# Kernel optimization log

Hardware: AMD Instinct MI355X
Metric: run time of the kernel (lower is better)

Reference implementation:

```python
import jax, jax.numpy as jnp
import numpy as np

B, C, P, GH, GW = 32, 3, 32, 8, 16
DIM, DEPTH, HEADS, DHEAD = 1024, 12, 16, 64
N = GH * GW              # 128 tokens
PATCH_DIM = C * P * P    # 3072
INNER = HEADS * DHEAD    # 1024
EPS = 1e-5


def layer_norm(x, g, b):
    mu = jnp.mean(x, axis=-1, keepdims=True)
    var = jnp.var(x, axis=-1, keepdims=True)
    return (x - mu) * jax.lax.rsqrt(var + EPS) * g + b


def setup_inputs() -> dict:
    key = jax.random.key(0)
    ks = iter(jax.random.split(key, 32))
    s = 0.02
    inp = {
        "img": jax.random.normal(next(ks), (B, C, GH * P, GW * P), jnp.float32),
        "sph_pos": jax.random.uniform(next(ks), (GH, GW, 2), jnp.float32),
        "sph_dist": jax.random.uniform(next(ks), (N, N), jnp.float32),
        # patch embedding conv (kernel == stride == patch)
        "conv_w": jax.random.normal(next(ks), (DIM, C, P, P), jnp.float32) * s,
        "conv_b": jnp.zeros((DIM,), jnp.float32),
        # norm_linear: LN -> Linear(dim,dim) -> LN
        "nl_ln1_g": jnp.ones((DIM,), jnp.float32),
        "nl_ln1_b": jnp.zeros((DIM,), jnp.float32),
        "nl_w": jax.random.normal(next(ks), (DIM, DIM), jnp.float32) * s,
        "nl_b": jnp.zeros((DIM,), jnp.float32),
        "nl_ln2_g": jnp.ones((DIM,), jnp.float32),
        "nl_ln2_b": jnp.zeros((DIM,), jnp.float32),
        # pos embedding Linear(2, dim)
        "pos_w": jax.random.normal(next(ks), (2, DIM), jnp.float32) * s,
        "pos_b": jnp.zeros((DIM,), jnp.float32),
        # per-layer attention params, stacked over depth
        "ln_g": jnp.ones((DEPTH, DIM), jnp.float32),
        "ln_b": jnp.zeros((DEPTH, DIM), jnp.float32),
        "wqkv": jax.random.normal(next(ks), (DEPTH, DIM, 3 * INNER), jnp.float32) * s,
        "wo": jax.random.normal(next(ks), (DEPTH, INNER, DIM), jnp.float32) * s,
        "wo_b": jnp.zeros((DEPTH, DIM), jnp.float32),
        # final transformer LN
        "tr_ln_g": jnp.ones((DIM,), jnp.float32),
        "tr_ln_b": jnp.zeros((DIM,), jnp.float32),
        # expand head: Linear(dim, patch_dim) + LN(patch_dim)
        "exp_w": jax.random.normal(next(ks), (DIM, PATCH_DIM), jnp.float32) * s,
        "exp_b": jnp.zeros((PATCH_DIM,), jnp.float32),
        "out_ln_g": jnp.ones((PATCH_DIM,), jnp.float32),
        "out_ln_b": jnp.zeros((PATCH_DIM,), jnp.float32),
    }
    return inp


def _forward(img, sph_pos, sph_dist, conv_w, conv_b, nl_ln1_g, nl_ln1_b, nl_w,
             nl_b, nl_ln2_g, nl_ln2_b, pos_w, pos_b, ln_g, ln_b, wqkv, wo,
             wo_b, tr_ln_g, tr_ln_b, exp_w, exp_b, out_ln_g, out_ln_b):
    b = img.shape[0]
    scale = DHEAD ** -0.5
    # patch embedding: Conv2d(kernel=stride=P) == per-patch linear
    patches = img.reshape(b, C, GH, P, GW, P)  # b c h p w q
    x = jnp.einsum('bchpwq,dcpq->bhwd', patches, conv_w) + conv_b  # [b,GH,GW,dim]
    x = x.reshape(b, N, DIM)
    # norm_linear
    x = layer_norm(x, nl_ln1_g, nl_ln1_b)
    x = x @ nl_w + nl_b
    x = layer_norm(x, nl_ln2_g, nl_ln2_b)
    # spherical positional embedding
    pos = (sph_pos @ pos_w + pos_b).reshape(N, DIM)
    x = x + pos[None]
    # transformer: GlobalSphereAttention blocks with residuals
    bias = 1.0 + sph_dist  # [N,N]
    for l in range(DEPTH):
        h = layer_norm(x, ln_g[l], ln_b[l])
        qkv = h @ wqkv[l]  # [b,n,3*inner]
        q, k, v = jnp.split(qkv, 3, axis=-1)
        q = q.reshape(b, N, HEADS, DHEAD).transpose(0, 2, 1, 3)
        k = k.reshape(b, N, HEADS, DHEAD).transpose(0, 2, 1, 3)
        v = v.reshape(b, N, HEADS, DHEAD).transpose(0, 2, 1, 3)
        dots = jnp.einsum('bhid,bhjd->bhij', q, k) * scale
        w = dots * bias  # broadcast over b,h
        # cross-head standardization (torch.std -> ddof=1)
        mu = jnp.mean(w, axis=1, keepdims=True)
        sd = jnp.std(w, axis=1, keepdims=True, ddof=1)
        attn = jax.nn.softmax((w - mu) / sd, axis=-1)
        o = jnp.einsum('bhij,bhjd->bhid', attn, v)
        o = o.transpose(0, 2, 1, 3).reshape(b, N, INNER)
        x = o @ wo[l] + wo_b[l] + x
    x = layer_norm(x, tr_ln_g, tr_ln_b)
    # expand and reassemble image: 'b (h w) (p1 p2 c) -> b c (h p1) (w p2)'
    x = layer_norm(x @ exp_w + exp_b, out_ln_g, out_ln_b)  # [b,N,patch_dim]
    x = x.reshape(b, GH, GW, P, P, C)
    x = x.transpose(0, 5, 1, 3, 2, 4).reshape(b, C, GH * P, GW * P)
    return x


def reference(img, sph_pos, sph_dist, conv_w, conv_b, nl_ln1_g, nl_ln1_b, nl_w,
              nl_b, nl_ln2_g, nl_ln2_b, pos_w, pos_b, ln_g, ln_b, wqkv, wo,
              wo_b, tr_ln_g, tr_ln_b, exp_w, exp_b, out_ln_g, out_ln_b):
    return _forward(img, sph_pos, sph_dist, conv_w, conv_b, nl_ln1_g, nl_ln1_b,
                    nl_w, nl_b, nl_ln2_g, nl_ln2_b, pos_w, pos_b, ln_g, ln_b,
                    wqkv, wo, wo_b, tr_ln_g, tr_ln_b, exp_w, exp_b, out_ln_g,
                    out_ln_b)
```

## Files before the change

kernel.cpp:

```cpp
#include <hip/hip_runtime.h>
#include <stdint.h>


typedef __attribute__((ext_vector_type(8))) short short8;
typedef __attribute__((ext_vector_type(4))) float f32x4;

#define EPS 1e-5f

__device__ __forceinline__ float b2f(ushort u) {
    union { uint32_t i; float f; } c; c.i = ((uint32_t)u) << 16; return c.f;
}
__device__ __forceinline__ ushort f2b(float f) {
    union { float f; uint32_t i; } c; c.f = f;
    uint32_t u = c.i;
    uint32_t r = (u + 0x7fffu + ((u >> 16) & 1u)) >> 16;
    return (ushort)r;
}
__device__ __forceinline__ void async16(const ushort* g, ushort* l) {
    __builtin_amdgcn_global_load_lds(
        (const __attribute__((address_space(1))) uint32_t*)g,
        (__attribute__((address_space(3))) uint32_t*)l, 16, 0, 0);
}

__device__ __forceinline__ float2 block_sum2(float s, float ss, int tid) {
    #pragma unroll
    for (int o = 32; o; o >>= 1) { s += __shfl_xor(s, o); ss += __shfl_xor(ss, o); }
    __shared__ float ps[4], pss[4];
    int w = tid >> 6;
    if ((tid & 63) == 0) { ps[w] = s; pss[w] = ss; }
    __syncthreads();
    return make_float2(ps[0] + ps[1] + ps[2] + ps[3],
                       pss[0] + pss[1] + pss[2] + pss[3]);
}

__global__ void sniff_dtype(const uint32_t* __restrict__ ones, int* __restrict__ flag) {
    if (threadIdx.x == 0 && blockIdx.x == 0) {
        int c32 = 0, c16 = 0;
        for (int i = 0; i < 256; i++) {
            uint32_t w = ones[i];
            c32 += (w == 0x3F800000u);
            c16 += (w == 0x3F803F80u);
        }
        *flag = (c32 >= c16) ? 1 : 0;
    }
}

template <int MODE>
__global__ __launch_bounds__(256) void gemm_nt(
    const ushort* __restrict__ A, const ushort* __restrict__ Bt,
    const void* __restrict__ bias, int bias_off, const int* __restrict__ flagp,
    float* __restrict__ Cf, ushort* __restrict__ Cb,
    int M, int N, int K, int ldA, int ldB, int ldC, int RM, int RN)
{
    __shared__ ushort As[128 * 32];
    __shared__ ushort Bs[128 * 32];
    const int tid = threadIdx.x, lane = tid & 63, w = tid >> 6;

    int lid = blockIdx.y * gridDim.x + blockIdx.x;
    int xcd = lid & 7, slot = lid >> 3;
    int regions_n = gridDim.x / RN;
    int r_m = xcd / regions_n, r_n = xcd % regions_n;
    int tm = r_m * RM + slot / RN;
    int tn = r_n * RN + slot % RN;
    const int m0 = tm * 128, n0 = tn * 128;

    const int wr = (w >> 1) * 64, wc = (w & 1) * 64;
    const int m16 = lane & 15, quad = lane >> 4;

    f32x4 acc[4][4];
    #pragma unroll
    for (int i = 0; i < 4; i++)
        #pragma unroll
        for (int j = 0; j < 4; j++) acc[i][j] = (f32x4){0.f, 0.f, 0.f, 0.f};

    const int idx0 = (w * 2) * 64 + lane, idx1 = (w * 2 + 1) * 64 + lane;
    const int row0 = idx0 >> 2, ks0 = (idx0 & 3) * 8;
    const int row1 = idx1 >> 2, ks1 = (idx1 & 3) * 8;
    const ushort* a0 = A  + (size_t)(m0 + row0) * ldA + ks0;
    const ushort* a1 = A  + (size_t)(m0 + row1) * ldA + ks1;
    const ushort* b0 = Bt + (size_t)(n0 + row0) * ldB + ks0;
    const ushort* b1 = Bt + (size_t)(n0 + row1) * ldB + ks1;

    for (int k0 = 0; k0 < K; k0 += 32) {
        __syncthreads();
        async16(a0 + k0, As + (w * 2 + 0) * 512);
        async16(a1 + k0, As + (w * 2 + 1) * 512);
        async16(b0 + k0, Bs + (w * 2 + 0) * 512);
        async16(b1 + k0, Bs + (w * 2 + 1) * 512);
        __syncthreads();
        short8 a[4], b[4];
        #pragma unroll
        for (int t = 0; t < 4; t++)
            a[t] = *(const short8*)(As + (wr + t * 16 + m16) * 32 + quad * 8);
        #pragma unroll
        for (int t = 0; t < 4; t++)
            b[t] = *(const short8*)(Bs + (wc + t * 16 + m16) * 32 + quad * 8);
        #pragma unroll
        for (int i = 0; i < 4; i++)
            #pragma unroll
            for (int j = 0; j < 4; j++)
                acc[i][j] = __builtin_amdgcn_mfma_f32_16x16x32_bf16(a[i], b[j], acc[i][j], 0, 0, 0);
    }

    float bvals[4] = {0.f, 0.f, 0.f, 0.f};
    if (bias) {
        if (*flagp) {
            #pragma unroll
            for (int j = 0; j < 4; j++)
                bvals[j] = ((const float*)bias)[bias_off + n0 + wc + j * 16 + m16];
        } else {
            #pragma unroll
            for (int j = 0; j < 4; j++)
                bvals[j] = b2f(((const ushort*)bias)[bias_off + n0 + wc + j * 16 + m16]);
        }
    }
    #pragma unroll
    for (int i = 0; i < 4; i++)
        #pragma unroll
        for (int j = 0; j < 4; j++)
            #pragma unroll
            for (int r = 0; r < 4; r++) {
                int row = m0 + wr + i * 16 + quad * 4 + r;
                int col = n0 + wc + j * 16 + m16;
                float v = acc[i][j][r] + bvals[j];
                if (MODE == 0)      Cf[(size_t)row * ldC + col] = v;
                else if (MODE == 1) Cb[(size_t)row * ldC + col] = f2b(v);
                else                Cf[(size_t)row * ldC + col] += v;
            }
}

__global__ __launch_bounds__(256) void transpose_k(
    const void* __restrict__ W, size_t eoff, ushort* __restrict__ Wt,
    int K, int N, const int* __restrict__ flagp)
{
    __shared__ ushort t[32][33];
    int f32 = *flagp;
    int n0 = blockIdx.x * 32, k0 = blockIdx.y * 32;
    int tx = threadIdx.x & 31, ty = threadIdx.x >> 5;
    if (f32) {
        const float* Wf = (const float*)W + eoff;
        #pragma unroll
        for (int i = ty; i < 32; i += 8) t[i][tx] = f2b(Wf[(size_t)(k0 + i) * N + n0 + tx]);
    } else {
        const ushort* Wb = (const ushort*)W + eoff;
        #pragma unroll
        for (int i = ty; i < 32; i += 8) t[i][tx] = Wb[(size_t)(k0 + i) * N + n0 + tx];
    }
    __syncthreads();
    #pragma unroll
    for (int i = ty; i < 32; i += 8) Wt[(size_t)(n0 + i) * K + k0 + tx] = t[tx][i];
}

__global__ __launch_bounds__(256) void convert_copy(
    const void* __restrict__ src, ushort* __restrict__ dst,
    const int* __restrict__ flagp)
{
    size_t i = ((size_t)blockIdx.x * 256 + threadIdx.x) * 8;
    if (*flagp) {
        const float* s = (const float*)src + i;
        ushort t[8];
        #pragma unroll
        for (int x = 0; x < 8; x++) t[x] = f2b(s[x]);
        *(uint4*)(dst + i) = *(uint4*)t;
    } else {
        *(uint4*)(dst + i) = *(const uint4*)((const ushort*)src + i);
    }
}

__global__ __launch_bounds__(256) void patch_gather(
    const void* __restrict__ img, ushort* __restrict__ Ap,
    const int* __restrict__ flagp)
{
    int t = blockIdx.x * 256 + threadIdx.x;
    int qc = t & 3;
    int p  = (t >> 2) & 31;
    int c  = (t >> 7) % 3;
    int rest = t / 384;
    int wg = rest & 15;
    int hg = (rest >> 4) & 7;
    int b  = rest >> 7;
    size_t si = ((size_t)((b * 3 + c) * 256 + hg * 32 + p)) * 512 + wg * 32 + qc * 8;
    size_t di = ((size_t)((b * 8 + hg) * 16 + wg)) * 3072 + c * 1024 + p * 32 + qc * 8;
    if (*flagp) {
        const float* s = (const float*)img + si;
        ushort tmp[8];
        #pragma unroll
        for (int x = 0; x < 8; x++) tmp[x] = f2b(s[x]);
        *(uint4*)(Ap + di) = *(uint4*)tmp;
    } else {
        *(uint4*)(Ap + di) = *(const uint4*)((const ushort*)img + si);
    }
}

__global__ __launch_bounds__(256) void ln_f32_to_bf16(
    const float* __restrict__ X, const void* __restrict__ g,
    const void* __restrict__ b, int goff, const int* __restrict__ flagp,
    ushort* __restrict__ Y)
{
    int row = blockIdx.x, tid = threadIdx.x;
    float4 v = ((const float4*)(X + (size_t)row * 1024))[tid];
    float s = v.x + v.y + v.z + v.w;
    float ss = v.x * v.x + v.y * v.y + v.z * v.z + v.w * v.w;
    float2 r = block_sum2(s, ss, tid);
    float mu = r.x * (1.f / 1024.f);
    float var = fmaxf(r.y * (1.f / 1024.f) - mu * mu, 0.f);
    float rs = rsqrtf(var + EPS);
    int c0 = tid * 4;
    float gv[4], bv[4];
    if (*flagp) {
        #pragma unroll
        for (int x = 0; x < 4; x++) { gv[x] = ((const float*)g)[goff + c0 + x]; bv[x] = ((const float*)b)[goff + c0 + x]; }
    } else {
        #pragma unroll
        for (int x = 0; x < 4; x++) { gv[x] = b2f(((const ushort*)g)[goff + c0 + x]); bv[x] = b2f(((const ushort*)b)[goff + c0 + x]); }
    }
    ushort4 o4;
    o4.x = f2b((v.x - mu) * rs * gv[0] + bv[0]);
    o4.y = f2b((v.y - mu) * rs * gv[1] + bv[1]);
    o4.z = f2b((v.z - mu) * rs * gv[2] + bv[2]);
    o4.w = f2b((v.w - mu) * rs * gv[3] + bv[3]);
    *(ushort4*)(Y + (size_t)row * 1024 + c0) = o4;
}

__global__ __launch_bounds__(256) void ln2_pos(
    float* __restrict__ X, const void* __restrict__ g, const void* __restrict__ b,
    const void* __restrict__ sph_pos, const void* __restrict__ pos_w,
    const void* __restrict__ pos_b, const int* __restrict__ flagp)
{
    int f32 = *flagp;
    int row = blockIdx.x, tid = threadIdx.x;
    float4 v = ((const float4*)(X + (size_t)row * 1024))[tid];
    float s = v.x + v.y + v.z + v.w;
    float ss = v.x * v.x + v.y * v.y + v.z * v.z + v.w * v.w;
    float2 r = block_sum2(s, ss, tid);
    float mu = r.x * (1.f / 1024.f);
    float var = fmaxf(r.y * (1.f / 1024.f) - mu * mu, 0.f);
    float rs = rsqrtf(var + EPS);
    int n = row & 127;
    int c0 = tid * 4;
    float s0, s1, gv[4], bv[4], w0[4], w1[4], pb[4];
    if (f32) {
        s0 = ((const float*)sph_pos)[n * 2 + 0]; s1 = ((const float*)sph_pos)[n * 2 + 1];
        #pragma unroll
        for (int x = 0; x < 4; x++) {
            gv[x] = ((const float*)g)[c0 + x];  bv[x] = ((const float*)b)[c0 + x];
            w0[x] = ((const float*)pos_w)[c0 + x]; w1[x] = ((const float*)pos_w)[1024 + c0 + x];
            pb[x] = ((const float*)pos_b)[c0 + x];
        }
    } else {
        s0 = b2f(((const ushort*)sph_pos)[n * 2 + 0]); s1 = b2f(((const ushort*)sph_pos)[n * 2 + 1]);
        #pragma unroll
        for (int x = 0; x < 4; x++) {
            gv[x] = b2f(((const ushort*)g)[c0 + x]);  bv[x] = b2f(((const ushort*)b)[c0 + x]);
            w0[x] = b2f(((const ushort*)pos_w)[c0 + x]); w1[x] = b2f(((const ushort*)pos_w)[1024 + c0 + x]);
            pb[x] = b2f(((const ushort*)pos_b)[c0 + x]);
        }
    }
    float4 o;
    o.x = (v.x - mu) * rs * gv[0] + bv[0] + s0 * w0[0] + s1 * w1[0] + pb[0];
    o.y = (v.y - mu) * rs * gv[1] + bv[1] + s0 * w0[1] + s1 * w1[1] + pb[1];
    o.z = (v.z - mu) * rs * gv[2] + bv[2] + s0 * w0[2] + s1 * w1[2] + pb[2];
    o.w = (v.w - mu) * rs * gv[3] + bv[3] + s0 * w0[3] + s1 * w1[3] + pb[3];
    *(float4*)(X + (size_t)row * 1024 + c0) = o;
}

__global__ __launch_bounds__(256) void attn_qk(
    const ushort* __restrict__ qkv, const void* __restrict__ sph_dist,
    const int* __restrict__ flagp, float* __restrict__ dots)
{
    __shared__ ushort Qs[128 * 64];
    __shared__ ushort Ks[128 * 64];
    int bh = blockIdx.x, b = bh >> 4, h = bh & 15;
    int tid = threadIdx.x;
    {
        int i = tid >> 1, half = (tid & 1) * 32;
        const ushort* qsrc = qkv + (size_t)(b * 128 + i) * 3072 + h * 64 + half;
        const ushort* ksrc = qsrc + 1024;
        uint4* qdst = (uint4*)(Qs + i * 64 + half);
        uint4* kdst = (uint4*)(Ks + i * 64 + half);
        #pragma unroll
        for (int x = 0; x < 4; x++) { qdst[x] = ((const uint4*)qsrc)[x]; kdst[x] = ((const uint4*)ksrc)[x]; }
    }
    __syncthreads();
    int lane = tid & 63, w = tid >> 6, m16 = lane & 15, quad = lane >> 4;
    f32x4 acc[2][8];
    #pragma unroll
    for (int i = 0; i < 2; i++)
        #pragma unroll
        for (int j = 0; j < 8; j++) acc[i][j] = (f32x4){0.f, 0.f, 0.f, 0.f};
    #pragma unroll
    for (int kq = 0; kq < 2; kq++) {
        short8 a[2], bb[8];
        #pragma unroll
        for (int rt = 0; rt < 2; rt++)
            a[rt] = *(const short8*)(Qs + (w * 32 + rt * 16 + m16) * 64 + kq * 32 + quad * 8);
        #pragma unroll
        for (int ct = 0; ct < 8; ct++)
            bb[ct] = *(const short8*)(Ks + (ct * 16 + m16) * 64 + kq * 32 + quad * 8);
        #pragma unroll
        for (int rt = 0; rt < 2; rt++)
            #pragma unroll
            for (int ct = 0; ct < 8; ct++)
                acc[rt][ct] = __builtin_amdgcn_mfma_f32_16x16x32_bf16(a[rt], bb[ct], acc[rt][ct], 0, 0, 0);
    }
    const float scale = 0.125f;
    int f32 = *flagp;
    #pragma unroll
    for (int rt = 0; rt < 2; rt++)
        #pragma unroll
        for (int ct = 0; ct < 8; ct++)
            #pragma unroll
            for (int r = 0; r < 4; r++) {
                int i = w * 32 + rt * 16 + quad * 4 + r;
                int j = ct * 16 + m16;
                float sd = f32 ? ((const float*)sph_dist)[i * 128 + j]
                               : b2f(((const ushort*)sph_dist)[i * 128 + j]);
                dots[((size_t)bh * 128 + i) * 128 + j] = acc[rt][ct][r] * scale * (1.f + sd);
            }
}

__global__ __launch_bounds__(256) void attn_stats(
    const float* __restrict__ dots, ushort* __restrict__ attn)
{
    int gi = blockIdx.x * 4 + (threadIdx.x >> 6);
    int lane = threadIdx.x & 63;
    int b = gi >> 7, i = gi & 127;
    float v0[16], v1[16];
    #pragma unroll
    for (int h = 0; h < 16; h++) {
        const float* p = dots + ((size_t)(b * 16 + h) * 128 + i) * 128;
        v0[h] = p[lane]; v1[h] = p[lane + 64];
    }
    float s0 = 0.f, s1 = 0.f;
    #pragma unroll
    for (int h = 0; h < 16; h++) { s0 += v0[h]; s1 += v1[h]; }
    float mu0 = s0 * (1.f / 16.f), mu1 = s1 * (1.f / 16.f);
    float q0 = 0.f, q1 = 0.f;
    #pragma unroll
    for (int h = 0; h < 16; h++) {
        float d0 = v0[h] - mu0, d1 = v1[h] - mu1;
        q0 += d0 * d0; q1 += d1 * d1;
    }
    float r0 = rsqrtf(fmaxf(q0 * (1.f / 15.f), 1e-20f));
    float r1 = rsqrtf(fmaxf(q1 * (1.f / 15.f), 1e-20f));
    #pragma unroll
    for (int h = 0; h < 16; h++) { v0[h] = (v0[h] - mu0) * r0; v1[h] = (v1[h] - mu1) * r1; }
    #pragma unroll
    for (int h = 0; h < 16; h++) {
        float m = fmaxf(v0[h], v1[h]);
        #pragma unroll
        for (int o = 32; o; o >>= 1) m = fmaxf(m, __shfl_xor(m, o));
        float e0 = __expf(v0[h] - m), e1 = __expf(v1[h] - m);
        float s = e0 + e1;
        #pragma unroll
        for (int o = 32; o; o >>= 1) s += __shfl_xor(s, o);
        float inv = 1.f / s;
        ushort* op = attn + ((size_t)(b * 16 + h) * 128 + i) * 128;
        op[lane] = f2b(e0 * inv);
        op[lane + 64] = f2b(e1 * inv);
    }
}

__global__ __launch_bounds__(256) void attn_pv(
    const ushort* __restrict__ attn, const ushort* __restrict__ qkv,
    ushort* __restrict__ o)
{
    __shared__ ushort Ps[128 * 128];
    __shared__ ushort Vt[64 * 128];
    int bh = blockIdx.x, b = bh >> 4, h = bh & 15;
    int tid = threadIdx.x;
    {
        int i = tid >> 1, jh = (tid & 1) * 64;
        const uint4* src = (const uint4*)(attn + ((size_t)bh * 128 + i) * 128 + jh);
        uint4* dst = (uint4*)(Ps + i * 128 + jh);
        #pragma unroll
        for (int x = 0; x < 8; x++) dst[x] = src[x];
    }
    {
        int j = tid >> 1, dh = (tid & 1) * 32;
        const ushort* src = qkv + (size_t)(b * 128 + j) * 3072 + 2048 + h * 64 + dh;
        ushort tmp[32];
        #pragma unroll
        for (int x = 0; x < 4; x++) *(uint4*)(tmp + x * 8) = ((const uint4*)src)[x];
        #pragma unroll
        for (int x = 0; x < 32; x++) Vt[(dh + x) * 128 + j] = tmp[x];
    }
    __syncthreads();
    int lane = tid & 63, w = tid >> 6, m16 = lane & 15, quad = lane >> 4;
    f32x4 acc[2][4];
    #pragma unroll
    for (int i = 0; i < 2; i++)
        #pragma unroll
        for (int j = 0; j < 4; j++) acc[i][j] = (f32x4){0.f, 0.f, 0.f, 0.f};
    #pragma unroll
    for (int kq = 0; kq < 4; kq++) {
        short8 a[2], bb[4];
        #pragma unroll
        for (int rt = 0; rt < 2; rt++)
            a[rt] = *(const short8*)(Ps + (w * 32 + rt * 16 + m16) * 128 + kq * 32 + quad * 8);
        #pragma unroll
        for (int ct = 0; ct < 4; ct++)
            bb[ct] = *(const short8*)(Vt + (ct * 16 + m16) * 128 + kq * 32 + quad * 8);
        #pragma unroll
        for (int rt = 0; rt < 2; rt++)
            #pragma unroll
            for (int ct = 0; ct < 4; ct++)
                acc[rt][ct] = __builtin_amdgcn_mfma_f32_16x16x32_bf16(a[rt], bb[ct], acc[rt][ct], 0, 0, 0);
    }
    #pragma unroll
    for (int rt = 0; rt < 2; rt++)
        #pragma unroll
        for (int ct = 0; ct < 4; ct++)
            #pragma unroll
            for (int r = 0; r < 4; r++) {
                int i = w * 32 + rt * 16 + quad * 4 + r;
                int d = ct * 16 + m16;
                o[(size_t)(b * 128 + i) * 1024 + h * 64 + d] = f2b(acc[rt][ct][r]);
            }
}

__global__ __launch_bounds__(256) void out_ln_rearrange(
    const ushort* __restrict__ Y, const void* __restrict__ g,
    const void* __restrict__ bb, const int* __restrict__ flagp,
    void* __restrict__ out)
{
    __shared__ float rowbuf[3072];
    int f32 = *flagp;
    int r = blockIdx.x;
    int b = r >> 7, n = r & 127, hg = n >> 4, wg = n & 15;
    int tid = threadIdx.x;
    float s = 0.f, ss = 0.f;
    #pragma unroll
    for (int x = 0; x < 3; x++) {
        ushort4 u = *(const ushort4*)(Y + (size_t)r * 3072 + (size_t)(x * 256 + tid) * 4);
        float4 v = make_float4(b2f(u.x), b2f(u.y), b2f(u.z), b2f(u.w));
        *(float4*)(rowbuf + (x * 256 + tid) * 4) = v;
        s += v.x + v.y + v.z + v.w;
        ss += v.x * v.x + v.y * v.y + v.z * v.z + v.w * v.w;
    }
    float2 red = block_sum2(s, ss, tid);
    float mu = red.x * (1.f / 3072.f);
    float var = fmaxf(red.y * (1.f / 3072.f) - mu * mu, 0.f);
    float rs = rsqrtf(var + EPS);
    int p1 = tid >> 3, sj = tid & 7;
    #pragma unroll
    for (int c = 0; c < 3; c++) {
        float vals[4];
        #pragma unroll
        for (int x = 0; x < 4; x++) {
            int p2 = sj * 4 + x;
            int col = p1 * 96 + p2 * 3 + c;
            float gv, bv;
            if (f32) { gv = ((const float*)g)[col];  bv = ((const float*)bb)[col]; }
            else     { gv = b2f(((const ushort*)g)[col]); bv = b2f(((const ushort*)bb)[col]); }
            vals[x] = (rowbuf[col] - mu) * rs * gv + bv;
        }
        size_t di = (size_t)((b * 3 + c) * 256 + hg * 32 + p1) * 512 + wg * 32 + sj * 4;
        if (f32) {
            *(float4*)((float*)out + di) = make_float4(vals[0], vals[1], vals[2], vals[3]);
        } else {
            ushort4 o4;
            #pragma unroll
            for (int x = 0; x < 4; x++) ((ushort*)&o4)[x] = f2b(vals[x]);
            *(ushort4*)((ushort*)out + di) = o4;
        }
    }
}

extern "C" void kernel_launch(void* const* d_in, const int* in_sizes, int n_in,
                              void* d_out, int out_size, void* d_ws, size_t ws_size,
                              hipStream_t stream)
{
    const void* img      = d_in[0];
    const void* sph_pos  = d_in[1];
    const void* sph_dist = d_in[2];
    const void* conv_w   = d_in[3];
    const void* conv_b   = d_in[4];
    const void* nl1g     = d_in[5];
    const void* nl1b     = d_in[6];
    const void* nl_w     = d_in[7];
    const void* nl_b     = d_in[8];
    const void* nl2g     = d_in[9];
    const void* nl2b     = d_in[10];
    const void* pos_w    = d_in[11];
    const void* pos_b    = d_in[12];
    const void* ln_g     = d_in[13];
    const void* ln_b     = d_in[14];
    const void* wqkv     = d_in[15];
    const void* wo       = d_in[16];
    const void* wo_b     = d_in[17];
    const void* trg      = d_in[18];
    const void* trb      = d_in[19];
    const void* exp_w    = d_in[20];
    const void* exp_b    = d_in[21];
    const void* og       = d_in[22];
    const void* ob       = d_in[23];

    char* ws = (char*)d_ws;
    float*  xf    = (float*) (ws + 0);
    ushort* xb    = (ushort*)(ws + 16777216);
    ushort* qkvb  = (ushort*)(ws + 25165824);
    float*  dots  = (float*) (ws + 50331648);
    float*  y1    = (float*) (ws + 50331648);
    ushort* o_bf  = (ushort*)(ws + 50331648);
    ushort* wTa   = (ushort*)(ws + 83886080);
    ushort* wTb   = (ushort*)(ws + 90177536);
    int*    flagp = (int*)   (ws + 92274688);
    ushort* attnb = (ushort*)d_out;

    sniff_dtype<<<1, 64, 0, stream>>>((const uint32_t*)nl1g, flagp);

    patch_gather<<<6144, 256, 0, stream>>>(img, qkvb, flagp);
    convert_copy<<<1536, 256, 0, stream>>>(conv_w, wTa, flagp);
    gemm_nt<0><<<dim3(8, 32), 256, 0, stream>>>(qkvb, wTa, conv_b, 0, flagp, y1, nullptr,
                                                4096, 1024, 3072, 3072, 3072, 1024, 4, 8);
    ln_f32_to_bf16<<<4096, 256, 0, stream>>>(y1, nl1g, nl1b, 0, flagp, xb);
    transpose_k<<<dim3(32, 32), 256, 0, stream>>>(nl_w, 0, wTb, 1024, 1024, flagp);
    gemm_nt<0><<<dim3(8, 32), 256, 0, stream>>>(xb, wTb, nl_b, 0, flagp, xf, nullptr,
                                                4096, 1024, 1024, 1024, 1024, 1024, 4, 8);
    ln2_pos<<<4096, 256, 0, stream>>>(xf, nl2g, nl2b, sph_pos, pos_w, pos_b, flagp);

    for (int l = 0; l < 12; l++) {
        transpose_k<<<dim3(96, 32), 256, 0, stream>>>(wqkv, (size_t)l * 1024 * 3072, wTa, 1024, 3072, flagp);
        transpose_k<<<dim3(32, 32), 256, 0, stream>>>(wo, (size_t)l * 1024 * 1024, wTb, 1024, 1024, flagp);
        ln_f32_to_bf16<<<4096, 256, 0, stream>>>(xf, ln_g, ln_b, l * 1024, flagp, xb);
        gemm_nt<1><<<dim3(24, 32), 256, 0, stream>>>(xb, wTa, nullptr, 0, flagp, nullptr, qkvb,
                                                     4096, 3072, 1024, 1024, 1024, 3072, 8, 12);
        attn_qk<<<512, 256, 0, stream>>>(qkvb, sph_dist, flagp, dots);
        attn_stats<<<1024, 256, 0, stream>>>(dots, attnb);
        attn_pv<<<512, 256, 0, stream>>>(attnb, qkvb, o_bf);
        gemm_nt<2><<<dim3(8, 32), 256, 0, stream>>>(o_bf, wTb, wo_b, l * 1024, flagp, xf, nullptr,
                                                    4096, 1024, 1024, 1024, 1024, 1024, 4, 8);
    }

    ln_f32_to_bf16<<<4096, 256, 0, stream>>>(xf, trg, trb, 0, flagp, xb);
    transpose_k<<<dim3(96, 32), 256, 0, stream>>>(exp_w, 0, wTa, 1024, 3072, flagp);
    gemm_nt<1><<<dim3(24, 32), 256, 0, stream>>>(xb, wTa, exp_b, 0, flagp, nullptr, qkvb,
                                                 4096, 3072, 1024, 1024, 1024, 3072, 8, 12);
    out_ln_rearrange<<<4096, 256, 0, stream>>>(qkvb, og, ob, flagp, d_out);
}
```

Measured before the change: 2.151 ms.

## Fuse QK, cross-head standardization softmax, and PV into one attention kernel

Replaces the three attention kernels (QK scores to global fp32, cross-head stats/softmax, PV) with one kernel per (batch, 16-query-row block) that keeps all 16 heads' scores in LDS. Cross-head mean/std, softmax and PV run from shared memory with XOR-swizzled bf16 packing, which removes the large fp32 dots and bf16 attn round trips through HBM and two launches per layer. In exchange only 256 blocks run with about 160KB of LDS each, so occupancy is low. Q/K/V are read straight from global memory without staging, with V reloaded per block.

```diff
diff --git a/kernel.cpp b/kernel.cpp
--- a/kernel.cpp
+++ b/kernel.cpp
@@ -15,6 +15,14 @@
     uint32_t u = c.i;
     uint32_t r = (u + 0x7fffu + ((u >> 16) & 1u)) >> 16;
     return (ushort)r;
+}
+__device__ __forceinline__ float pack2(ushort lo, ushort hi) {
+    union { uint32_t u; float f; } c;
+    c.u = (uint32_t)lo | ((uint32_t)hi << 16);
+    return c.f;
+}
+__device__ __forceinline__ short8 as_short8(f32x4 v) {
+    union { f32x4 f; short8 s; } u; u.f = v; return u.s;
 }
 __device__ __forceinline__ void async16(const ushort* g, ushort* l) {
     __builtin_amdgcn_global_load_lds(
@@ -264,159 +272,137 @@
     *(float4*)(X + (size_t)row * 1024 + c0) = o;
 }
 
-__global__ __launch_bounds__(256) void attn_qk(
+__global__ __launch_bounds__(256) void attn_fused(
     const ushort* __restrict__ qkv, const void* __restrict__ sph_dist,
-    const int* __restrict__ flagp, float* __restrict__ dots)
-{
-    __shared__ ushort Qs[128 * 64];
-    __shared__ ushort Ks[128 * 64];
-    int bh = blockIdx.x, b = bh >> 4, h = bh & 15;
-    int tid = threadIdx.x;
-    {
-        int i = tid >> 1, half = (tid & 1) * 32;
-        const ushort* qsrc = qkv + (size_t)(b * 128 + i) * 3072 + h * 64 + half;
-        const ushort* ksrc = qsrc + 1024;
-        uint4* qdst = (uint4*)(Qs + i * 64 + half);
-        uint4* kdst = (uint4*)(Ks + i * 64 + half);
-        #pragma unroll
-        for (int x = 0; x < 4; x++) { qdst[x] = ((const uint4*)qsrc)[x]; kdst[x] = ((const uint4*)ksrc)[x]; }
+    const int* __restrict__ flagp, ushort* __restrict__ o)
+{
+    __shared__ float dotsf[16 * 16 * 128];
+    __shared__ float musd[16 * 128 * 2];
+    const int tid = threadIdx.x, lane = tid & 63, w = tid >> 6;
+    const int m16 = lane & 15, quad = lane >> 4;
+    const int b = blockIdx.x & 31, i0 = (blockIdx.x >> 5) * 16;
+    const int f32 = *flagp;
+
+    float sphm[8][4];
+    #pragma unroll
+    for (int ct = 0; ct < 8; ct++)
+        #pragma unroll
+        for (int r = 0; r < 4; r++) {
+            int i = i0 + quad * 4 + r, j = ct * 16 + m16;
+            float sd = f32 ? ((const float*)sph_dist)[i * 128 + j]
+                           : b2f(((const ushort*)sph_dist)[i * 128 + j]);
+            sphm[ct][r] = 0.125f * (1.f + sd);
+        }
+
+    const ushort* qrow = qkv + (size_t)(b * 128 + i0 + m16) * 3072 + quad * 8;
+    const ushort* krow = qkv + (size_t)(b * 128 + m16) * 3072 + 1024 + quad * 8;
+    #pragma unroll
+    for (int hh = 0; hh < 4; hh++) {
+        const int h = w * 4 + hh;
+        short8 qa0 = *(const short8*)(qrow + h * 64);
+        short8 qa1 = *(const short8*)(qrow + h * 64 + 32);
+        f32x4 acc[8];
+        #pragma unroll
+        for (int ct = 0; ct < 8; ct++) acc[ct] = (f32x4){0.f, 0.f, 0.f, 0.f};
+        #pragma unroll
+        for (int ct = 0; ct < 8; ct++) {
+            const ushort* kp = krow + (size_t)ct * 16 * 3072 + h * 64;
+            short8 k0 = *(const short8*)(kp);
+            short8 k1 = *(const short8*)(kp + 32);
+            acc[ct] = __builtin_amdgcn_mfma_f32_16x16x32_bf16(qa0, k0, acc[ct], 0, 0, 0);
+            acc[ct] = __builtin_amdgcn_mfma_f32_16x16x32_bf16(qa1, k1, acc[ct], 0, 0, 0);
+        }
+        #pragma unroll
+        for (int ct = 0; ct < 8; ct++)
+            #pragma unroll
+            for (int r = 0; r < 4; r++)
+                dotsf[h * 2048 + (quad * 4 + r) * 128 + ct * 16 + m16] =
+                    acc[ct][r] * sphm[ct][r];
     }
     __syncthreads();
-    int lane = tid & 63, w = tid >> 6, m16 = lane & 15, quad = lane >> 4;
-    f32x4 acc[2][8];
-    #pragma unroll
-    for (int i = 0; i < 2; i++)
-        #pragma unroll
-        for (int j = 0; j < 8; j++) acc[i][j] = (f32x4){0.f, 0.f, 0.f, 0.f};
-    #pragma unroll
-    for (int kq = 0; kq < 2; kq++) {
-        short8 a[2], bb[8];
-        #pragma unroll
-        for (int rt = 0; rt < 2; rt++)
-            a[rt] = *(const short8*)(Qs + (w * 32 + rt * 16 + m16) * 64 + kq * 32 + quad * 8);
-        #pragma unroll
-        for (int ct = 0; ct < 8; ct++)
-            bb[ct] = *(const short8*)(Ks + (ct * 16 + m16) * 64 + kq * 32 + quad * 8);
-        #pragma unroll
-        for (int rt = 0; rt < 2; rt++)
-            #pragma unroll
-            for (int ct = 0; ct < 8; ct++)
-                acc[rt][ct] = __builtin_amdgcn_mfma_f32_16x16x32_bf16(a[rt], bb[ct], acc[rt][ct], 0, 0, 0);
-    }
-    const float scale = 0.125f;
-    int f32 = *flagp;
-    #pragma unroll
-    for (int rt = 0; rt < 2; rt++)
-        #pragma unroll
-        for (int ct = 0; ct < 8; ct++)
-            #pragma unroll
-            for (int r = 0; r < 4; r++) {
-                int i = w * 32 + rt * 16 + quad * 4 + r;
-                int j = ct * 16 + m16;
-                float sd = f32 ? ((const float*)sph_dist)[i * 128 + j]
-                               : b2f(((const ushort*)sph_dist)[i * 128 + j]);
-                dots[((size_t)bh * 128 + i) * 128 + j] = acc[rt][ct][r] * scale * (1.f + sd);
+
+    #pragma unroll
+    for (int p = 0; p < 8; p++) {
+        int idx = p * 256 + tid, i = idx >> 7, j = idx & 127;
+        float v[16], s = 0.f;
+        #pragma unroll
+        for (int h = 0; h < 16; h++) { v[h] = dotsf[h * 2048 + i * 128 + j]; s += v[h]; }
+        float mu = s * (1.f / 16.f), q = 0.f;
+        #pragma unroll
+        for (int h = 0; h < 16; h++) { float d = v[h] - mu; q += d * d; }
+        float rsd = rsqrtf(fmaxf(q * (1.f / 15.f), 1e-20f));
+        musd[(i * 128 + j) * 2]     = mu;
+        musd[(i * 128 + j) * 2 + 1] = rsd;
+    }
+    __syncthreads();
+
+    #pragma unroll
+    for (int hh = 0; hh < 4; hh++) {
+        const int h = w * 4 + hh;
+        #pragma unroll
+        for (int i = 0; i < 16; i++) {
+            float x0 = dotsf[h * 2048 + i * 128 + 2 * lane];
+            float x1 = dotsf[h * 2048 + i * 128 + 2 * lane + 1];
+            float4 ms = *(const float4*)&musd[i * 256 + 4 * lane];
+            x0 = (x0 - ms.x) * ms.y;
+            x1 = (x1 - ms.z) * ms.w;
+            float m = fmaxf(x0, x1);
+            #pragma unroll
+            for (int o2 = 32; o2; o2 >>= 1) m = fmaxf(m, __shfl_xor(m, o2));
+            float e0 = __expf(x0 - m), e1 = __expf(x1 - m);
+            float s = e0 + e1;
+            #pragma unroll
+            for (int o2 = 32; o2; o2 >>= 1) s += __shfl_xor(s, o2);
+            float inv = 1.f / s;
+            dotsf[h * 2048 + i * 64 + (lane ^ ((i & 7) << 2))] =
+                pack2(f2b(e0 * inv), f2b(e1 * inv));
+        }
+    }
+    __syncthreads();
+
+    #pragma unroll 1
+    for (int g = 0; g < 4; g++) {
+        const int h = w * 4 + g;
+        {
+            const ushort* vr0 = qkv + (size_t)(b * 128 + 2 * lane) * 3072 + 2048 + h * 64;
+            const ushort* vr1 = vr0 + 3072;
+            short8 r0[8], r1[8];
+            #pragma unroll
+            for (int x = 0; x < 8; x++) {
+                r0[x] = *(const short8*)(vr0 + x * 8);
+                r1[x] = *(const short8*)(vr1 + x * 8);
             }
-}
-
-__global__ __launch_bounds__(256) void attn_stats(
-    const float* __restrict__ dots, ushort* __restrict__ attn)
-{
-    int gi = blockIdx.x * 4 + (threadIdx.x >> 6);
-    int lane = threadIdx.x & 63;
-    int b = gi >> 7, i = gi & 127;
-    float v0[16], v1[16];
-    #pragma unroll
-    for (int h = 0; h < 16; h++) {
-        const float* p = dots + ((size_t)(b * 16 + h) * 128 + i) * 128;
-        v0[h] = p[lane]; v1[h] = p[lane + 64];
-    }
-    float s0 = 0.f, s1 = 0.f;
-    #pragma unroll
-    for (int h = 0; h < 16; h++) { s0 += v0[h]; s1 += v1[h]; }
-    float mu0 = s0 * (1.f / 16.f), mu1 = s1 * (1.f / 16.f);
-    float q0 = 0.f, q1 = 0.f;
-    #pragma unroll
-    for (int h = 0; h < 16; h++) {
-        float d0 = v0[h] - mu0, d1 = v1[h] - mu1;
-        q0 += d0 * d0; q1 += d1 * d1;
-    }
-    float r0 = rsqrtf(fmaxf(q0 * (1.f / 15.f), 1e-20f));
-    float r1 = rsqrtf(fmaxf(q1 * (1.f / 15.f), 1e-20f));
-    #pragma unroll
-    for (int h = 0; h < 16; h++) { v0[h] = (v0[h] - mu0) * r0; v1[h] = (v1[h] - mu1) * r1; }
-    #pragma unroll
-    for (int h = 0; h < 16; h++) {
-        float m = fmaxf(v0[h], v1[h]);
-        #pragma unroll
-        for (int o = 32; o; o >>= 1) m = fmaxf(m, __shfl_xor(m, o));
-        float e0 = __expf(v0[h] - m), e1 = __expf(v1[h] - m);
-        float s = e0 + e1;
-        #pragma unroll
-        for (int o = 32; o; o >>= 1) s += __shfl_xor(s, o);
-        float inv = 1.f / s;
-        ushort* op = attn + ((size_t)(b * 16 + h) * 128 + i) * 128;
-        op[lane] = f2b(e0 * inv);
-        op[lane + 64] = f2b(e1 * inv);
-    }
-}
-
-__global__ __launch_bounds__(256) void attn_pv(
-    const ushort* __restrict__ attn, const ushort* __restrict__ qkv,
-    ushort* __restrict__ o)
-{
-    __shared__ ushort Ps[128 * 128];
-    __shared__ ushort Vt[64 * 128];
-    int bh = blockIdx.x, b = bh >> 4, h = bh & 15;
-    int tid = threadIdx.x;
-    {
-        int i = tid >> 1, jh = (tid & 1) * 64;
-        const uint4* src = (const uint4*)(attn + ((size_t)bh * 128 + i) * 128 + jh);
-        uint4* dst = (uint4*)(Ps + i * 128 + jh);
-        #pragma unroll
-        for (int x = 0; x < 8; x++) dst[x] = src[x];
-    }
-    {
-        int j = tid >> 1, dh = (tid & 1) * 32;
-        const ushort* src = qkv + (size_t)(b * 128 + j) * 3072 + 2048 + h * 64 + dh;
-        ushort tmp[32];
-        #pragma unroll
-        for (int x = 0; x < 4; x++) *(uint4*)(tmp + x * 8) = ((const uint4*)src)[x];
-        #pragma unroll
-        for (int x = 0; x < 32; x++) Vt[(dh + x) * 128 + j] = tmp[x];
-    }
-    __syncthreads();
-    int lane = tid & 63, w = tid >> 6, m16 = lane & 15, quad = lane >> 4;
-    f32x4 acc[2][4];
-    #pragma unroll
-    for (int i = 0; i < 2; i++)
-        #pragma unroll
-        for (int j = 0; j < 4; j++) acc[i][j] = (f32x4){0.f, 0.f, 0.f, 0.f};
-    #pragma unroll
-    for (int kq = 0; kq < 4; kq++) {
-        short8 a[2], bb[4];
-        #pragma unroll
-        for (int rt = 0; rt < 2; rt++)
-            a[rt] = *(const short8*)(Ps + (w * 32 + rt * 16 + m16) * 128 + kq * 32 + quad * 8);
+            #pragma unroll
+            for (int d = 0; d < 64; d++)
+                dotsf[(w * 4 + (d >> 4)) * 2048 + 1024 + (d & 15) * 64 +
+                      (lane ^ ((d & 7) << 2))] =
+                    pack2((ushort)r0[d >> 3][d & 7], (ushort)r1[d >> 3][d & 7]);
+        }
+        __syncthreads();
+        f32x4 pacc[4];
+        #pragma unroll
+        for (int ct = 0; ct < 4; ct++) pacc[ct] = (f32x4){0.f, 0.f, 0.f, 0.f};
+        const int sw = (m16 & 7) << 2;
+        #pragma unroll
+        for (int kq = 0; kq < 4; kq++) {
+            f32x4 paw = *(const f32x4*)&dotsf[h * 2048 + m16 * 64 +
+                                              ((kq * 16 + quad * 4) ^ sw)];
+            short8 pa = as_short8(paw);
+            #pragma unroll
+            for (int ct = 0; ct < 4; ct++) {
+                f32x4 vbw = *(const f32x4*)&dotsf[(w * 4 + ct) * 2048 + 1024 + m16 * 64 +
+                                                  ((kq * 16 + quad * 4) ^ sw)];
+                pacc[ct] = __builtin_amdgcn_mfma_f32_16x16x32_bf16(pa, as_short8(vbw), pacc[ct], 0, 0, 0);
+            }
+        }
         #pragma unroll
         for (int ct = 0; ct < 4; ct++)
-            bb[ct] = *(const short8*)(Vt + (ct * 16 + m16) * 128 + kq * 32 + quad * 8);
-        #pragma unroll
-        for (int rt = 0; rt < 2; rt++)
-            #pragma unroll
-            for (int ct = 0; ct < 4; ct++)
-                acc[rt][ct] = __builtin_amdgcn_mfma_f32_16x16x32_bf16(a[rt], bb[ct], acc[rt][ct], 0, 0, 0);
-    }
-    #pragma unroll
-    for (int rt = 0; rt < 2; rt++)
-        #pragma unroll
-        for (int ct = 0; ct < 4; ct++)
-            #pragma unroll
-            for (int r = 0; r < 4; r++) {
-                int i = w * 32 + rt * 16 + quad * 4 + r;
-                int d = ct * 16 + m16;
-                o[(size_t)(b * 128 + i) * 1024 + h * 64 + d] = f2b(acc[rt][ct][r]);
-            }
+            #pragma unroll
+            for (int r = 0; r < 4; r++)
+                o[(size_t)(b * 128 + i0 + quad * 4 + r) * 1024 + h * 64 + ct * 16 + m16] =
+                    f2b(pacc[ct][r]);
+        __syncthreads();
+    }
 }
 
 __global__ __launch_bounds__(256) void out_ln_rearrange(
@@ -500,13 +486,11 @@
     float*  xf    = (float*) (ws + 0);
     ushort* xb    = (ushort*)(ws + 16777216);
     ushort* qkvb  = (ushort*)(ws + 25165824);
-    float*  dots  = (float*) (ws + 50331648);
     float*  y1    = (float*) (ws + 50331648);
     ushort* o_bf  = (ushort*)(ws + 50331648);
     ushort* wTa   = (ushort*)(ws + 83886080);
     ushort* wTb   = (ushort*)(ws + 90177536);
     int*    flagp = (int*)   (ws + 92274688);
-    ushort* attnb = (ushort*)d_out;
 
     sniff_dtype<<<1, 64, 0, stream>>>((const uint32_t*)nl1g, flagp);
 
@@ -526,9 +510,7 @@
         ln_f32_to_bf16<<<4096, 256, 0, stream>>>(xf, ln_g, ln_b, l * 1024, flagp, xb);
         gemm_nt<1><<<dim3(24, 32), 256, 0, stream>>>(xb, wTa, nullptr, 0, flagp, nullptr, qkvb,
                                                      4096, 3072, 1024, 1024, 1024, 3072, 8, 12);
-        attn_qk<<<512, 256, 0, stream>>>(qkvb, sph_dist, flagp, dots);
-        attn_stats<<<1024, 256, 0, stream>>>(dots, attnb);
-        attn_pv<<<512, 256, 0, stream>>>(attnb, qkvb, o_bf);
+        attn_fused<<<256, 256, 0, stream>>>(qkvb, sph_dist, flagp, o_bf);
         gemm_nt<2><<<dim3(8, 32), 256, 0, stream>>>(o_bf, wTb, wo_b, l * 1024, flagp, xf, nullptr,
                                                     4096, 1024, 1024, 1024, 1024, 1024, 4, 8);
     }
```

Result: no change. 2.179 ms (+1.3%).
